# Kernel optimization log

Measured on AMD Instinct MI355X. Metric: run time of the kernel, lower is better.

## Reference

```python
import jax, jax.numpy as jnp
import numpy as np
import math


def _ln(x, g, b):
    mu = jnp.mean(x, -1, keepdims=True)
    var = jnp.mean((x - mu) ** 2, -1, keepdims=True)
    return (x - mu) / jnp.sqrt(var + 1e-5) * g + b


def _gelu(x):
    # torch nn.GELU default = exact erf form
    return jax.nn.gelu(x, approximate=False)


def _prm_exp(x, w):
    # FAVOR+ positive random features: exp(w x - |x|^2/2) / sqrt(m)
    m = w.shape[0]
    xd = jnp.sum(x * x, axis=-1, keepdims=True) * 0.5  # (B,T,1)
    wtx = jnp.einsum('btd,md->btm', x, w)
    return jnp.exp(wtx - xd) / math.sqrt(m)


def setup_inputs() -> dict:
    key = jax.random.key(0)
    ks = jax.random.split(key, 8)
    B, T = 16, 3136
    Cin, D = 768, 384
    m = int(D * 0.5)  # kernel_ratio = 0.5 -> 192 random features
    s = lambda fan_in: 1.0 / np.sqrt(fan_in)
    inp = {
        'input_1': jax.random.normal(ks[0], (B, T, Cin // 2), jnp.float32),
        'input_2': jax.random.normal(ks[1], (B, T, Cin // 2), jnp.float32),
        'W1': jax.random.uniform(ks[2], (Cin, D), jnp.float32, -s(Cin), s(Cin)),
        'b1': jnp.zeros((D,), jnp.float32),
        'W2': jax.random.uniform(ks[3], (D, D), jnp.float32, -s(D), s(D)),
        'b2': jnp.zeros((D,), jnp.float32),
        'kqv_w': jax.random.uniform(ks[4], (D, 3 * D), jnp.float32, -s(D), s(D)),
        'kqv_b': jnp.zeros((3 * D,), jnp.float32),
        'proj_w': jax.random.uniform(ks[5], (D, D), jnp.float32, -s(D), s(D)),
        'proj_b': jnp.zeros((D,), jnp.float32),
        'ln1_g': jnp.ones((D,), jnp.float32),
        'ln1_b': jnp.zeros((D,), jnp.float32),
        'ln2_g': jnp.ones((D,), jnp.float32),
        'ln2_b': jnp.zeros((D,), jnp.float32),
        'mlp_w1': jax.random.uniform(ks[6], (D, D), jnp.float32, -s(D), s(D)),
        'mlp_b1': jnp.zeros((D,), jnp.float32),
        'mlp_w2': jax.random.uniform(ks[7], (D, D), jnp.float32, -s(D), s(D)),
        'mlp_b2': jnp.zeros((D,), jnp.float32),
    }
    # frozen orthogonal projection (m, D) scaled by sqrt(m), as in Token_performer
    g = np.random.default_rng(0).standard_normal((D, m)).astype(np.float32)
    q, _ = np.linalg.qr(g)  # (D, m) orthonormal columns
    inp['w_prm'] = jnp.asarray((q.T * math.sqrt(m)).astype(np.float32))  # (m, D)
    return inp


def reference(input_1, input_2, W1, b1, W2, b2, kqv_w, kqv_b, proj_w, proj_b,
              ln1_g, ln1_b, ln2_g, ln2_b, mlp_w1, mlp_b1, mlp_w2, mlp_b2, w_prm):
    # concatFuse: Linear -> GELU -> Linear
    x = jnp.concatenate([input_1, input_2], axis=2)
    x = _gelu(x @ W1 + b1) @ W2 + b2  # (B, T, D)

    # Token_performer (dropout = identity in eval)
    xn = _ln(x, ln1_g, ln1_b)
    kqv = xn @ kqv_w + kqv_b
    k, q, v = jnp.split(kqv, 3, axis=-1)  # torch.split order: k, q, v
    kp = _prm_exp(k, w_prm)  # (B, T, m)
    qp = _prm_exp(q, w_prm)  # (B, T, m)
    Dn = jnp.einsum('btm,bm->bt', qp, kp.sum(axis=1))[..., None]  # (B, T, 1)
    kptv = jnp.einsum('btd,btm->bdm', v, kp)  # (B, D, m)
    y = jnp.einsum('btm,bdm->btd', qp, kptv) / (Dn + 1e-8)  # (B, T, D)
    y = v + (y @ proj_w + proj_b)  # residual is v, per Token_performer

    z = _ln(y, ln2_g, ln2_b)
    h = _gelu(z @ mlp_w1 + mlp_b1) @ mlp_w2 + mlp_b2
    return y + h
```

## Files before the change

### kernel.cpp

```cpp
#include <hip/hip_runtime.h>
#include <math.h>

typedef unsigned short u16;
typedef unsigned int   u32;
typedef __attribute__((ext_vector_type(8))) short short8;
typedef __attribute__((ext_vector_type(4))) float f32x4;

typedef const void __attribute__((address_space(1))) gvoid_t;
typedef void       __attribute__((address_space(3))) svoid_t;

__device__ __forceinline__ void gload_lds16(const void* g, void* l){
    __builtin_amdgcn_global_load_lds((gvoid_t*)g, (svoid_t*)l, 16, 0, 0);
}

__device__ __forceinline__ float gelu_f(float x){
    return 0.5f * x * (1.0f + erff(x * 0.70710678118654752f));
}
__device__ __forceinline__ u16 f2b(float x){
    union{float f; u32 u;} v; v.f = x;
    u32 r = (v.u + 0x7fffu + ((v.u >> 16) & 1u)) >> 16;
    return (u16)r;
}
__device__ __forceinline__ float b2f(u16 h){
    union{u32 u; float f;} v; v.u = ((u32)h) << 16; return v.f;
}

template<int EPI, int GUARD, int CGUARD>
__global__ __launch_bounds__(256)
void gemm_bf16(const u16* __restrict__ A, int lda,
               const u16* __restrict__ B, int ldb,
               void* __restrict__ Cv, int ldc,
               const float* __restrict__ bias,
               const float* __restrict__ rowv,
               void* __restrict__ resid, int ldr,
               int Mrows, int Ncols, int K, int splitK,
               long sA, long sB, long sC, long sRV,
               float scale)
{
    const int bz = blockIdx.z;
    const int b  = bz / splitK, kc = bz % splitK;
    A += (long)b * sA;  B += (long)b * sB;
    const float* rv = (EPI == 3) ? rowv + (long)b * sRV : nullptr;

    __shared__ u16 SMEM[16384];
    __shared__ float xds[128];
    u16* const As = SMEM;
    u16* const Bs = SMEM + 8192;

    const int tid = threadIdx.x;

    const int gx  = gridDim.x;
    const int nwg = gx * gridDim.y;
    const int L   = blockIdx.y * gx + blockIdx.x;
    const int q8  = nwg >> 3, r8 = nwg & 7;
    const int xc  = L & 7,   i8 = L >> 3;
    const int nid = (xc < r8 ? xc * (q8 + 1) : r8 * (q8 + 1) + (xc - r8) * q8) + i8;
    const int row0 = (nid / gx) * 128, col0 = (nid % gx) * 128;

    f32x4 acc[4][4] = {};
    float sqacc[4] = {0.f, 0.f, 0.f, 0.f};

    const int l  = tid & 63, w4 = tid >> 6;
    const int wr = w4 >> 1, wc = w4 & 1;
    const int g  = l >> 4,  mr = l & 15;

    const int kLen   = K / splitK;
    const int kStart = kc * kLen;
    const int nt     = kLen / 64;

    const int m0   = w4 * 8 + (l >> 3);
    const int k8s  = (l & 7) ^ (m0 & 7);
    const int lBase = w4 * 512 + l * 8;
    const u16* gA0 = A + (long)(row0 + m0) * lda + kStart + k8s * 8;
    const u16* gB0 = B + (long)(col0 + m0) * ldb + kStart + k8s * 8;

    int aOff[4], bOff[4], sl[2];
    #pragma unroll
    for (int i = 0; i < 4; i++){
        aOff[i] = (wr * 64 + i * 16 + mr) * 64;
        bOff[i] = (wc * 64 + i * 16 + mr) * 64;
    }
    #pragma unroll
    for (int kk = 0; kk < 2; kk++)
        sl[kk] = (((kk * 4 + g) ^ (mr & 7)) & 7) * 8;

    for (int t = 0; t < nt; t++){
        __syncthreads();
        #pragma unroll
        for (int q = 0; q < 4; q++){
            gload_lds16(gA0 + (long)q * 32 * lda + t * 64, &As[lBase + q * 2048]);
            gload_lds16(gB0 + (long)q * 32 * ldb + t * 64, &Bs[lBase + q * 2048]);
        }
        __syncthreads();

        short8 af[2][4], bfr[2][4];
        #pragma unroll
        for (int kk = 0; kk < 2; kk++)
            #pragma unroll
            for (int i = 0; i < 4; i++){
                af[kk][i]  = *(const short8*)&As[aOff[i] + sl[kk]];
                bfr[kk][i] = *(const short8*)&Bs[bOff[i] + sl[kk]];
            }
        if (EPI == 10){
            #pragma unroll
            for (int kk = 0; kk < 2; kk++)
                #pragma unroll
                for (int i = 0; i < 4; i++)
                    #pragma unroll
                    for (int e = 0; e < 8; e++){
                        float f_ = b2f((u16)af[kk][i][e]);
                        sqacc[i] += f_ * f_;
                    }
        }
        #pragma unroll
        for (int kk = 0; kk < 2; kk++)
            #pragma unroll
            for (int i = 0; i < 4; i++)
                #pragma unroll
                for (int j = 0; j < 4; j++)
                    acc[i][j] = __builtin_amdgcn_mfma_f32_16x16x32_bf16(af[kk][i], bfr[kk][j], acc[i][j], 0, 0, 0);
    }

    if (EPI == 10){
        #pragma unroll
        for (int i = 0; i < 4; i++){
            float s = sqacc[i];
            s += __shfl_xor(s, 16);
            s += __shfl_xor(s, 32);
            if (l < 16) xds[wr * 64 + i * 16 + l] = 0.5f * s;
        }
    }
    __syncthreads();

    float* Cf = (float*)Cv + (long)b * sC;
    u16*   Cb = (u16*)Cv   + (EPI == 10 ? 0L : (EPI == 8 ? (long)bz : (long)b) * sC);

    if (EPI == 10 && bz == 0){
        #pragma unroll
        for (int i = 0; i < 4; i++){
            #pragma unroll
            for (int j = 0; j < 4; j++){
                const int col = col0 + wc * 64 + j * 16 + mr;
                if (CGUARD && col >= Ncols) continue;
                const int lrow = wr * 64 + i * 16 + g * 4;
                u16 pk[4];
                #pragma unroll
                for (int r = 0; r < 4; r++)
                    pk[r] = f2b(expf(acc[i][j][r] - xds[lrow + r]) * scale);
                *(ushort4*)&Cb[(long)col * ldc + row0 + lrow] = *(ushort4*)pk;
            }
        }
        return;
    }

    if (EPI == 9){
        #pragma unroll
        for (int i = 0; i < 4; i++){
            #pragma unroll
            for (int j = 0; j < 4; j++){
                const int col = col0 + wc * 64 + j * 16 + mr;
                if (CGUARD && col >= Ncols) continue;
                const float bv = bias[col];
                #pragma unroll
                for (int r = 0; r < 4; r++){
                    const int row = row0 + wr * 64 + i * 16 + g * 4 + r;
                    if (GUARD && row >= Mrows) continue;
                    const float vv = acc[i][j][r] + bv
                        + b2f(((const u16*)resid)[(long)row * ldr + col]);
                    Cf[(long)row * ldc + col] = vv;
                }
            }
        }
        return;
    }

    #pragma unroll
    for (int i = 0; i < 4; i++){
        #pragma unroll
        for (int j = 0; j < 4; j++){
            const int cl = wc * 64 + j * 16 + mr;
            const float bv = (EPI == 0 || EPI == 1 || EPI == 11)
                           ? bias[col0 + cl] : 0.f;
            #pragma unroll
            for (int r = 0; r < 4; r++){
                const int rl = wr * 64 + i * 16 + g * 4 + r;
                float vv = acc[i][j][r];
                if      (EPI == 1)  vv = gelu_f(vv + bv);
                else if (EPI == 3)  vv = vv / (rv[row0 + rl] + 1e-8f);
                else if (EPI == 10) vv = expf(vv - xds[rl]) * scale;
                else                vv += bv;
                SMEM[rl * 128 + cl] = f2b(vv);
            }
        }
    }
    __syncthreads();

    u16* dst; long ld;
    if (EPI == 10){ dst = (u16*)resid; ld = ldr; }
    else          { dst = Cb;          ld = ldc; }
    #pragma unroll
    for (int s = 0; s < 8; s++){
        const int oi = s * 256 + tid;
        const int rl = oi >> 4, c8 = (oi & 15) << 3;
        const int row = row0 + rl, col = col0 + c8;
        if (GUARD && row >= Mrows) continue;
        if (CGUARD && col >= Ncols) continue;
        uint4 pv = *(uint4*)&SMEM[rl * 128 + c8];
        if (EPI == 11){
            const u16* rp = (const u16*)resid + (long)row * ldr + col;
            uint4 rv4 = *(const uint4*)rp;
            u16* a = (u16*)&pv; const u16* c = (const u16*)&rv4;
            #pragma unroll
            for (int e = 0; e < 8; e++) a[e] = f2b(b2f(a[e]) + b2f(c[e]));
        }
        *(uint4*)&dst[(long)row * ld + col] = pv;
    }
}

__global__ __launch_bounds__(256)
void trb_kernel(const u16* __restrict__ in, long inStride, u16* __restrict__ out, long R)
{
    __shared__ u16 t[64][72];
    const long cb = (long)blockIdx.x * 64, rb = (long)blockIdx.y * 64;
    const int tl = threadIdx.x & 63, tw = threadIdx.x >> 6;
    #pragma unroll
    for (int i = 0; i < 16; i++){
        const int r = tw + i * 4;
        t[r][tl] = in[(rb + r) * inStride + cb + tl];
    }
    __syncthreads();
    #pragma unroll
    for (int i = 0; i < 16; i++){
        const int c = tw + i * 4;
        out[(cb + c) * R + rb + tl] = t[tl][c];
    }
}

__global__ __launch_bounds__(256)
void kred_kernel(const u16* __restrict__ in, u16* __restrict__ out, long n)
{
    long idx = (long)blockIdx.x * 256 + threadIdx.x;
    if (idx >= n) return;
    const long b = idx / 73728, r = idx - b * 73728;
    const u16* s = in + b * 7 * 73728L + r;
    float acc = 0.f;
    #pragma unroll
    for (int kc = 0; kc < 7; kc++) acc += b2f(s[kc * 73728L]);
    out[idx] = f2b(acc);
}

template<int INF32>
__global__ __launch_bounds__(256)
void ln_kernel(const void* __restrict__ xv, u16* __restrict__ ob,
               const float* __restrict__ g, const float* __restrict__ bta)
{
    const int lane = threadIdx.x & 63;
    const long r = (long)blockIdx.x * 4 + (threadIdx.x >> 6);
    float v[6]; float s = 0.f;
    #pragma unroll
    for (int i = 0; i < 6; i++){
        const int c = lane + i * 64;
        v[i] = INF32 ? ((const float*)xv)[r * 384 + c]
                     : b2f(((const u16*)xv)[r * 384 + c]);
        s += v[i];
    }
    #pragma unroll
    for (int off = 32; off; off >>= 1) s += __shfl_xor(s, off);
    const float mu = s * (1.0f/384.0f);
    float q = 0.f;
    #pragma unroll
    for (int i = 0; i < 6; i++){ float d = v[i] - mu; q += d*d; }
    #pragma unroll
    for (int off = 32; off; off >>= 1) q += __shfl_xor(q, off);
    const float inv = rsqrtf(q * (1.0f/384.0f) + 1e-5f);
    #pragma unroll
    for (int i = 0; i < 6; i++){
        const int c = lane + i*64;
        ob[r * 384 + c] = f2b((v[i] - mu) * inv * g[c] + bta[c]);
    }
}

__global__ __launch_bounds__(256)
void dn_kernel(const u16* __restrict__ qp, const float* __restrict__ kpsum,
               float* __restrict__ Dn, int T)
{
    const int lane = threadIdx.x & 63;
    const long r = (long)blockIdx.x * 4 + (threadIdx.x >> 6);
    const int b = (int)(r / T);
    const u16* qr = qp + r * 192;
    const float* ks = kpsum + (long)b * 192;
    float s = 0.f;
    #pragma unroll
    for (int i = 0; i < 3; i++){ const int m = lane + i*64; s += b2f(qr[m]) * ks[m]; }
    #pragma unroll
    for (int off = 32; off; off >>= 1) s += __shfl_xor(s, off);
    if (lane == 0) Dn[r] = s;
}

__global__ __launch_bounds__(256)
void kpsum2_kernel(const u16* __restrict__ kpT, float* __restrict__ kpsum, long Mc, int T)
{
    const int lane = threadIdx.x & 63;
    const int gw = blockIdx.x * 4 + (threadIdx.x >> 6);
    const int m = gw % 192, bl = gw / 192;
    const u16* row = kpT + (long)m * Mc + (long)bl * T;
    float s = 0.f;
    for (int i = lane; i < T; i += 64) s += b2f(row[i]);
    #pragma unroll
    for (int off = 32; off; off >>= 1) s += __shfl_xor(s, off);
    if (lane == 0) kpsum[bl * 192 + m] = s;
}

__global__ __launch_bounds__(256)
void zero_kernel(float* __restrict__ p, long n)
{
    long i = (long)blockIdx.x * 256 + threadIdx.x;
    long stride = (long)gridDim.x * 256;
    for (; i < n; i += stride) p[i] = 0.f;
}

__global__ __launch_bounds__(256)
void ca_kernel(const float* __restrict__ i1, const float* __restrict__ i2,
               u16* __restrict__ a0, long nquad)
{
    long idx = (long)blockIdx.x * 256 + threadIdx.x;
    if (idx >= nquad) return;
    const long r = idx / 192;
    const int  c0 = (int)(idx % 192) * 4;
    const float* src = (c0 < 384) ? &i1[r * 384 + c0] : &i2[r * 384 + (c0 - 384)];
    float4 v = *(const float4*)src;
    u32 w0 = (u32)f2b(v.x) | ((u32)f2b(v.y) << 16);
    u32 w1 = (u32)f2b(v.z) | ((u32)f2b(v.w) << 16);
    *(uint2*)&a0[r * 768 + c0] = make_uint2(w0, w1);
}

__global__ __launch_bounds__(256)
void wt_kernel(const float* __restrict__ w, u16* __restrict__ wt, int K, int N, long total)
{
    long idx = (long)blockIdx.x * 256 + threadIdx.x;
    if (idx >= total) return;
    const long n = idx / K, k = idx - n * K;
    wt[idx] = f2b(w[k * N + n]);
}

__global__ __launch_bounds__(256)
void cvt_kernel(const float* __restrict__ s, u16* __restrict__ d, long n4)
{
    long idx = (long)blockIdx.x * 256 + threadIdx.x;
    if (idx >= n4) return;
    float4 v = *(const float4*)&s[idx * 4];
    u32 w0 = (u32)f2b(v.x) | ((u32)f2b(v.y) << 16);
    u32 w1 = (u32)f2b(v.z) | ((u32)f2b(v.w) << 16);
    *(uint2*)&d[idx * 4] = make_uint2(w0, w1);
}

extern "C" void kernel_launch(void* const* d_in, const int* in_sizes, int n_in,
                              void* d_out, int out_size, void* d_ws, size_t ws_size,
                              hipStream_t stream)
{
    const long T = 3136;
    const float prm_scale = 0.07216878364870322f;

    const float* in1    = (const float*)d_in[0];
    const float* in2    = (const float*)d_in[1];
    const float* W1     = (const float*)d_in[2];
    const float* b1     = (const float*)d_in[3];
    const float* W2     = (const float*)d_in[4];
    const float* b2     = (const float*)d_in[5];
    const float* kqv_w  = (const float*)d_in[6];
    const float* kqv_b  = (const float*)d_in[7];
    const float* proj_w = (const float*)d_in[8];
    const float* proj_b = (const float*)d_in[9];
    const float* ln1_g  = (const float*)d_in[10];
    const float* ln1_b  = (const float*)d_in[11];
    const float* ln2_g  = (const float*)d_in[12];
    const float* ln2_b  = (const float*)d_in[13];
    const float* mlp_w1 = (const float*)d_in[14];
    const float* mlp_b1 = (const float*)d_in[15];
    const float* mlp_w2 = (const float*)d_in[16];
    const float* mlp_b2 = (const float*)d_in[17];
    const float* w_prm  = (const float*)d_in[18];
    float* out = (float*)d_out;

    char* p = (char*)d_ws;
    auto alloc = [&](long bytes)->char*{ char* r = p; p += (bytes + 255) & ~255L; return r; };

    u16* w1t   = (u16*)alloc(294912L * 2);
    u16* w2t   = (u16*)alloc(147456L * 2);
    u16* kqvt  = (u16*)alloc(442368L * 2);
    u16* prjt  = (u16*)alloc(147456L * 2);
    u16* m1t   = (u16*)alloc(147456L * 2);
    u16* m2t   = (u16*)alloc(147456L * 2);
    u16* wprmb = (u16*)alloc(256L * 384 * 2);
    char* chunkBase = p;

    const long perBatch = 2368L * T * 2 + T * 4
                        + 192L * 4 + 7L * 73728 * 2 + 73728L * 2;
    const long fixed = (long)(chunkBase - (char*)d_ws) + (1L << 20);
    int nb = 2;
    for (int cand = 16; cand >= 2; cand >>= 1){
        if (fixed + (long)cand * perBatch + 128L * 1024 <= (long)ws_size){ nb = cand; break; }
    }

    const dim3 blk(256);

    wt_kernel<<<dim3((294912 + 255) / 256), blk, 0, stream>>>(W1, w1t, 768, 384, 294912);
    wt_kernel<<<dim3((147456 + 255) / 256), blk, 0, stream>>>(W2, w2t, 384, 384, 147456);
    wt_kernel<<<dim3((442368 + 255) / 256), blk, 0, stream>>>(kqv_w, kqvt, 384, 1152, 442368);
    wt_kernel<<<dim3((147456 + 255) / 256), blk, 0, stream>>>(proj_w, prjt, 384, 384, 147456);
    wt_kernel<<<dim3((147456 + 255) / 256), blk, 0, stream>>>(mlp_w1, m1t, 384, 384, 147456);
    wt_kernel<<<dim3((147456 + 255) / 256), blk, 0, stream>>>(mlp_w2, m2t, 384, 384, 147456);
    zero_kernel<<<dim3(64), blk, 0, stream>>>((float*)wprmb, 256L * 384 / 2);
    cvt_kernel<<<dim3((18432 + 255) / 256), blk, 0, stream>>>(w_prm, wprmb, 18432);

    for (int b0 = 0; b0 < 16; b0 += nb){
        const long Mc = (long)nb * T;
        const int  gy128 = (int)(Mc / 128);
        const float* i1 = in1 + (long)b0 * T * 384;
        const float* i2 = in2 + (long)b0 * T * 384;
        float* outc = out + (long)b0 * T * 384;

        p = chunkBase;
        u16*  big   = (u16*)alloc(Mc * 1152 * 2);
        u16*  xb    = (u16*)alloc(Mc * 384 * 2);
        u16*  qpb   = (u16*)alloc(Mc * 192 * 2);
        u16*  vT    = (u16*)alloc(384L * Mc * 2);
        u16*  kpT   = (u16*)alloc(256L * Mc * 2);
        float* Dn   = (float*)alloc(Mc * 4);
        float* kpsum= (float*)alloc((long)nb * 192 * 4);
        u16*  kptvA = (u16*)alloc((long)nb * 7 * 73728 * 2);
        u16*  kptvb = (u16*)alloc((long)nb * 73728 * 2);
        (void)alloc(128L * 1024);

        u16* a0   = big;
        u16* h1   = big + Mc * 768;
        u16* kqvb = big;
        u16* hbuf = big;
        u16* ybf  = vT;

        {
            long nq = Mc * 192;
            ca_kernel<<<dim3((unsigned)((nq + 255) / 256)), blk, 0, stream>>>(i1, i2, a0, nq);
        }
        gemm_bf16<1,0,0><<<dim3(3, gy128, 1), blk, 0, stream>>>(
            a0, 768, w1t, 768, h1, 384, b1, nullptr, nullptr, 0,
            (int)Mc, 384, 768, 1, 0,0,0,0, 0.f);
        gemm_bf16<0,0,0><<<dim3(3, gy128, 1), blk, 0, stream>>>(
            h1, 384, w2t, 384, xb, 384, b2, nullptr, nullptr, 0,
            (int)Mc, 384, 384, 1, 0,0,0,0, 0.f);
        ln_kernel<0><<<dim3((unsigned)(Mc / 4)), blk, 0, stream>>>(xb, xb, ln1_g, ln1_b);
        gemm_bf16<0,0,0><<<dim3(9, gy128, 1), blk, 0, stream>>>(
            xb, 384, kqvt, 384, kqvb, 1152, kqv_b, nullptr, nullptr, 0,
            (int)Mc, 1152, 384, 1, 0,0,0,0, 0.f);
        gemm_bf16<10,0,1><<<dim3(2, gy128, 2), blk, 0, stream>>>(
            kqvb, 1152, wprmb, 384, kpT, (int)Mc, nullptr, nullptr, qpb, 192,
            (int)Mc, 192, 384, 1, 384, 0, 0, 0, prm_scale);
        kpsum2_kernel<<<dim3(nb * 48), blk, 0, stream>>>(kpT, kpsum, Mc, (int)T);
        trb_kernel<<<dim3(6, (unsigned)(Mc / 64)), blk, 0, stream>>>(kqvb + 768, 1152, vT, Mc);
        gemm_bf16<8,0,1><<<dim3(2, 3, nb * 7), blk, 0, stream>>>(
            vT, (int)Mc, kpT, (int)Mc, kptvA, 192, nullptr, nullptr, nullptr, 0,
            384, 192, 3136, 7, 3136, 3136, 73728, 0, 0.f);
        kred_kernel<<<dim3((unsigned)((long)nb * 73728 / 256)), blk, 0, stream>>>(
            kptvA, kptvb, (long)nb * 73728);
        dn_kernel<<<dim3((unsigned)(Mc / 4)), blk, 0, stream>>>(qpb, kpsum, Dn, (int)T);
        gemm_bf16<3,1,0><<<dim3(3, 25, nb), blk, 0, stream>>>(
            qpb, 192, kptvb, 192, xb, 384, nullptr, Dn, nullptr, 0,
            (int)T, 384, 192, 1, T*192, 73728, T*384, T, 0.f);
        gemm_bf16<11,0,0><<<dim3(3, gy128, 1), blk, 0, stream>>>(
            xb, 384, prjt, 384, ybf, 384, proj_b, nullptr, kqvb + 768, 1152,
            (int)Mc, 384, 384, 1, 0,0,0,0, 0.f);
        ln_kernel<0><<<dim3((unsigned)(Mc / 4)), blk, 0, stream>>>(ybf, xb, ln2_g, ln2_b);
        gemm_bf16<1,0,0><<<dim3(3, gy128, 1), blk, 0, stream>>>(
            xb, 384, m1t, 384, hbuf, 384, mlp_b1, nullptr, nullptr, 0,
            (int)Mc, 384, 384, 1, 0,0,0,0, 0.f);
        gemm_bf16<9,0,0><<<dim3(3, gy128, 1), blk, 0, stream>>>(
            hbuf, 384, m2t, 384, outc, 384, mlp_b2, nullptr, ybf, 384,
            (int)Mc, 384, 384, 1, 0,0,0,0, 0.f);
    }
}
```

Baseline: 534.5 us.

## Fuse input concat/convert into first GEMM and V transpose into KQV epilogue

Adds a dedicated first-layer GEMM that reads the two fp32 inputs directly, converts them to bf16 in registers and stores them into LDS. This removes the separate concat/convert kernel and its bf16 intermediate round trip. The KQV GEMM gets a new epilogue variant that also writes the V columns transposed into vT, which removes the standalone transpose kernel. The trade-off is synchronous global A loads in the new GEMM with no global-to-LDS async path, plus scattered 8-byte transposed stores in the epilogue.

```diff
diff --git a/kernel.cpp b/kernel.cpp
--- a/kernel.cpp
+++ b/kernel.cpp
@@ -179,8 +179,9 @@
         #pragma unroll
         for (int j = 0; j < 4; j++){
             const int cl = wc * 64 + j * 16 + mr;
-            const float bv = (EPI == 0 || EPI == 1 || EPI == 11)
+            const float bv = (EPI == 0 || EPI == 1 || EPI == 11 || EPI == 12)
                            ? bias[col0 + cl] : 0.f;
+            u16 pk[4];
             #pragma unroll
             for (int r = 0; r < 4; r++){
                 const int rl = wr * 64 + i * 16 + g * 4 + r;
@@ -189,7 +190,13 @@
                 else if (EPI == 3)  vv = vv / (rv[row0 + rl] + 1e-8f);
                 else if (EPI == 10) vv = expf(vv - xds[rl]) * scale;
                 else                vv += bv;
-                SMEM[rl * 128 + cl] = f2b(vv);
+                pk[r] = f2b(vv);
+                SMEM[rl * 128 + cl] = pk[r];
+            }
+            if (EPI == 12 && col0 >= 768){
+                const int lrow = wr * 64 + i * 16 + g * 4;
+                u16* vt = (u16*)resid;
+                *(ushort4*)&vt[(long)(col0 + cl - 768) * ldr + row0 + lrow] = *(ushort4*)pk;
             }
         }
     }
@@ -218,21 +225,106 @@
 }
 
 __global__ __launch_bounds__(256)
-void trb_kernel(const u16* __restrict__ in, long inStride, u16* __restrict__ out, long R)
-{
-    __shared__ u16 t[64][72];
-    const long cb = (long)blockIdx.x * 64, rb = (long)blockIdx.y * 64;
-    const int tl = threadIdx.x & 63, tw = threadIdx.x >> 6;
-    #pragma unroll
-    for (int i = 0; i < 16; i++){
-        const int r = tw + i * 4;
-        t[r][tl] = in[(rb + r) * inStride + cb + tl];
+void gemm_f1(const float* __restrict__ i1, const float* __restrict__ i2,
+             const u16* __restrict__ B, u16* __restrict__ C,
+             const float* __restrict__ bias)
+{
+    __shared__ u16 SMEM[16384];
+    u16* const As = SMEM;
+    u16* const Bs = SMEM + 8192;
+
+    const int tid = threadIdx.x;
+
+    const int gx  = gridDim.x;
+    const int nwg = gx * gridDim.y;
+    const int L   = blockIdx.y * gx + blockIdx.x;
+    const int q8  = nwg >> 3, r8 = nwg & 7;
+    const int xc  = L & 7,   i8 = L >> 3;
+    const int nid = (xc < r8 ? xc * (q8 + 1) : r8 * (q8 + 1) + (xc - r8) * q8) + i8;
+    const int row0 = (nid / gx) * 128, col0 = (nid % gx) * 128;
+
+    f32x4 acc[4][4] = {};
+
+    const int l  = tid & 63, w4 = tid >> 6;
+    const int wr = w4 >> 1, wc = w4 & 1;
+    const int g  = l >> 4,  mr = l & 15;
+
+    const int m0   = w4 * 8 + (l >> 3);
+    const int k8s  = (l & 7) ^ (m0 & 7);
+    const int lBase = w4 * 512 + l * 8;
+    const u16* gB0 = B + (long)(col0 + m0) * 768 + k8s * 8;
+
+    int aOff[4], bOff[4], sl[2];
+    #pragma unroll
+    for (int i = 0; i < 4; i++){
+        aOff[i] = (wr * 64 + i * 16 + mr) * 64;
+        bOff[i] = (wc * 64 + i * 16 + mr) * 64;
+    }
+    #pragma unroll
+    for (int kk = 0; kk < 2; kk++)
+        sl[kk] = (((kk * 4 + g) ^ (mr & 7)) & 7) * 8;
+
+    for (int t = 0; t < 12; t++){
+        const float* src = (t < 6) ? i1 : i2;
+        const int kt = (t < 6 ? t : t - 6) * 64;
+        float4 ra[4][2];
+        #pragma unroll
+        for (int q = 0; q < 4; q++){
+            const float* sp = src + (long)(row0 + q * 32 + m0) * 384 + kt + k8s * 8;
+            ra[q][0] = *(const float4*)sp;
+            ra[q][1] = *(const float4*)(sp + 4);
+        }
+        __syncthreads();
+        #pragma unroll
+        for (int q = 0; q < 4; q++){
+            uint4 pk;
+            pk.x = (u32)f2b(ra[q][0].x) | ((u32)f2b(ra[q][0].y) << 16);
+            pk.y = (u32)f2b(ra[q][0].z) | ((u32)f2b(ra[q][0].w) << 16);
+            pk.z = (u32)f2b(ra[q][1].x) | ((u32)f2b(ra[q][1].y) << 16);
+            pk.w = (u32)f2b(ra[q][1].z) | ((u32)f2b(ra[q][1].w) << 16);
+            *(uint4*)&As[lBase + q * 2048] = pk;
+            gload_lds16(gB0 + (long)q * 32 * 768 + t * 64, &Bs[lBase + q * 2048]);
+        }
+        __syncthreads();
+
+        short8 af[2][4], bfr[2][4];
+        #pragma unroll
+        for (int kk = 0; kk < 2; kk++)
+            #pragma unroll
+            for (int i = 0; i < 4; i++){
+                af[kk][i]  = *(const short8*)&As[aOff[i] + sl[kk]];
+                bfr[kk][i] = *(const short8*)&Bs[bOff[i] + sl[kk]];
+            }
+        #pragma unroll
+        for (int kk = 0; kk < 2; kk++)
+            #pragma unroll
+            for (int i = 0; i < 4; i++)
+                #pragma unroll
+                for (int j = 0; j < 4; j++)
+                    acc[i][j] = __builtin_amdgcn_mfma_f32_16x16x32_bf16(af[kk][i], bfr[kk][j], acc[i][j], 0, 0, 0);
     }
     __syncthreads();
-    #pragma unroll
-    for (int i = 0; i < 16; i++){
-        const int c = tw + i * 4;
-        out[(cb + c) * R + rb + tl] = t[tl][c];
+
+    #pragma unroll
+    for (int i = 0; i < 4; i++){
+        #pragma unroll
+        for (int j = 0; j < 4; j++){
+            const int cl = wc * 64 + j * 16 + mr;
+            const float bv = bias[col0 + cl];
+            #pragma unroll
+            for (int r = 0; r < 4; r++){
+                const int rl = wr * 64 + i * 16 + g * 4 + r;
+                SMEM[rl * 128 + cl] = f2b(gelu_f(acc[i][j][r] + bv));
+            }
+        }
+    }
+    __syncthreads();
+
+    #pragma unroll
+    for (int s = 0; s < 8; s++){
+        const int oi = s * 256 + tid;
+        const int rl = oi >> 4, c8 = (oi & 15) << 3;
+        *(uint4*)&C[(long)(row0 + rl) * 384 + col0 + c8] = *(uint4*)&SMEM[rl * 128 + c8];
     }
 }
 
@@ -317,21 +409,6 @@
     long i = (long)blockIdx.x * 256 + threadIdx.x;
     long stride = (long)gridDim.x * 256;
     for (; i < n; i += stride) p[i] = 0.f;
-}
-
-__global__ __launch_bounds__(256)
-void ca_kernel(const float* __restrict__ i1, const float* __restrict__ i2,
-               u16* __restrict__ a0, long nquad)
-{
-    long idx = (long)blockIdx.x * 256 + threadIdx.x;
-    if (idx >= nquad) return;
-    const long r = idx / 192;
-    const int  c0 = (int)(idx % 192) * 4;
-    const float* src = (c0 < 384) ? &i1[r * 384 + c0] : &i2[r * 384 + (c0 - 384)];
-    float4 v = *(const float4*)src;
-    u32 w0 = (u32)f2b(v.x) | ((u32)f2b(v.y) << 16);
-    u32 w1 = (u32)f2b(v.z) | ((u32)f2b(v.w) << 16);
-    *(uint2*)&a0[r * 768 + c0] = make_uint2(w0, w1);
 }
 
 __global__ __launch_bounds__(256)
@@ -432,31 +509,23 @@
         u16*  kptvb = (u16*)alloc((long)nb * 73728 * 2);
         (void)alloc(128L * 1024);
 
-        u16* a0   = big;
         u16* h1   = big + Mc * 768;
         u16* kqvb = big;
         u16* hbuf = big;
         u16* ybf  = vT;
 
-        {
-            long nq = Mc * 192;
-            ca_kernel<<<dim3((unsigned)((nq + 255) / 256)), blk, 0, stream>>>(i1, i2, a0, nq);
-        }
-        gemm_bf16<1,0,0><<<dim3(3, gy128, 1), blk, 0, stream>>>(
-            a0, 768, w1t, 768, h1, 384, b1, nullptr, nullptr, 0,
-            (int)Mc, 384, 768, 1, 0,0,0,0, 0.f);
+        gemm_f1<<<dim3(3, gy128, 1), blk, 0, stream>>>(i1, i2, w1t, h1, b1);
         gemm_bf16<0,0,0><<<dim3(3, gy128, 1), blk, 0, stream>>>(
             h1, 384, w2t, 384, xb, 384, b2, nullptr, nullptr, 0,
             (int)Mc, 384, 384, 1, 0,0,0,0, 0.f);
         ln_kernel<0><<<dim3((unsigned)(Mc / 4)), blk, 0, stream>>>(xb, xb, ln1_g, ln1_b);
-        gemm_bf16<0,0,0><<<dim3(9, gy128, 1), blk, 0, stream>>>(
-            xb, 384, kqvt, 384, kqvb, 1152, kqv_b, nullptr, nullptr, 0,
+        gemm_bf16<12,0,0><<<dim3(9, gy128, 1), blk, 0, stream>>>(
+            xb, 384, kqvt, 384, kqvb, 1152, kqv_b, nullptr, vT, (int)Mc,
             (int)Mc, 1152, 384, 1, 0,0,0,0, 0.f);
         gemm_bf16<10,0,1><<<dim3(2, gy128, 2), blk, 0, stream>>>(
             kqvb, 1152, wprmb, 384, kpT, (int)Mc, nullptr, nullptr, qpb, 192,
             (int)Mc, 192, 384, 1, 384, 0, 0, 0, prm_scale);
         kpsum2_kernel<<<dim3(nb * 48), blk, 0, stream>>>(kpT, kpsum, Mc, (int)T);
-        trb_kernel<<<dim3(6, (unsigned)(Mc / 64)), blk, 0, stream>>>(kqvb + 768, 1152, vT, Mc);
         gemm_bf16<8,0,1><<<dim3(2, 3, nb * 7), blk, 0, stream>>>(
             vT, (int)Mc, kpT, (int)Mc, kptvA, 192, nullptr, nullptr, nullptr, 0,
             384, 192, 3136, 7, 3136, 3136, 73728, 0, 0.f);
```

Result: no change. 537.4 us (+0.6%).
